# Optimization experiments

Measured on AMD Instinct MI355X. Metric: run time of the kernel, lower is better.

The kernel has to match this reference:

```python
import jax, jax.numpy as jnp
import numpy as np
from jax import lax

B, T, H = 64, 1024, 512
K = 10            # gaussian mixtures
U, V = 64, 80     # char steps, alphabet size
S = 3             # stroke dims


def setup_inputs() -> dict:
    key = jax.random.key(0)
    k1, k2, k3, k4 = jax.random.split(key, 4)
    return {
        "input0": jax.random.normal(k1, (B, T, H), dtype=jnp.float32),
        "stroke": jax.random.normal(k2, (B, T, S), dtype=jnp.float32),
        "char": jax.random.uniform(k3, (B, U, V), dtype=jnp.float32),
        "window_w": jax.random.normal(k4, (H, 3 * K), dtype=jnp.float32) * 0.05,
        "window_b": jnp.zeros((3 * K,), dtype=jnp.float32),
        "kappa0": jnp.zeros((B, K, 1), dtype=jnp.float32),
    }


def reference(input0, stroke, char, window_w, window_b, kappa0):
    u = jnp.arange(char.shape[1], dtype=input0.dtype)  # [U]
    k_mix = kappa0.shape[1]

    def step(kappa_prev, xs):
        x_t, s_t = xs  # [B,H], [B,S]
        abk = jnp.exp(x_t @ window_w + window_b)          # [B,3K]
        abk = abk.reshape(-1, 3 * k_mix, 1)               # [B,3K,1]
        alpha, beta, kappa_hat = jnp.split(abk, 3, axis=1)  # each [B,K,1]
        kappa = kappa_hat + kappa_prev                    # cumulative kappa state
        # phi_k = alpha * exp(-beta * (kappa - u)^2) -> sum over mixtures
        phi = jnp.sum(alpha * jnp.exp(-beta * jnp.square(kappa - u)), axis=1)  # [B,U]
        window = jnp.einsum('bu,buv->bv', phi, char)      # [B,V]
        out = jnp.concatenate((x_t, window, s_t), axis=1)  # [B,H+V+S]
        return kappa, out

    xs = (jnp.swapaxes(input0, 0, 1), jnp.swapaxes(stroke, 0, 1))  # [T,B,*]
    _, outs = lax.scan(step, kappa0, xs)
    return jnp.swapaxes(outs, 0, 1)  # [B,T,H+V+S]
```

## Files before the change

### kernel.cpp

```cpp
#include <hip/hip_runtime.h>

#define BB 64
#define TT 1024
#define HH 512
#define KMIX 10
#define UU 64
#define VV 80
#define SDIM 3
#define OUTW (HH + VV + SDIM)
#define ROWS 16

__global__ __launch_bounds__(256) void kW_transpose(const float* __restrict__ Wm, float* __restrict__ Wt) {
    int idx = blockIdx.x * 256 + threadIdx.x;
    if (idx < 30 * HH) {
        int j = idx >> 9, h = idx & 511;
        Wt[idx] = Wm[h * 30 + j];
    }
}

__global__ __launch_bounds__(512, 4) void k1_gemm(
    const float* __restrict__ x,
    const float* __restrict__ stroke,
    const float* __restrict__ Wt,
    const float* __restrict__ bias,
    float* __restrict__ out,
    float* __restrict__ abk)
{
    __shared__ float xs[ROWS][HH + 4];
    const int tid = threadIdx.x;
    const int r0 = blockIdx.x * ROWS;

    const float4* x4 = (const float4*)(x + (size_t)r0 * HH);
    #pragma unroll
    for (int i = 0; i < 4; ++i) {
        int f4 = tid + (i << 9);
        float4 v = x4[f4];
        *(float4*)&xs[f4 >> 7][(f4 & 127) << 2] = v;
    }
    if (tid < ROWS * SDIM) {
        int row = tid / SDIM, c = tid % SDIM;
        out[(size_t)(r0 + row) * OUTW + HH + VV + c] = stroke[(size_t)(r0 + row) * SDIM + c];
    }
    __syncthreads();

    #pragma unroll
    for (int i = 0; i < 16; ++i) {
        int idx = tid + (i << 9);
        out[(size_t)(r0 + (idx >> 9)) * OUTW + (idx & 511)] = xs[idx >> 9][idx & 511];
    }

    const bool active = tid < 480;
    float acc[ROWS];
    int j = 0, hc = 0;
    if (active) {
        hc = tid / 30;
        j = tid % 30;
        const float4* wp = (const float4*)(Wt + j * HH + hc * 32);
        float4 w4[8];
        #pragma unroll
        for (int q = 0; q < 8; ++q) w4[q] = wp[q];
        #pragma unroll
        for (int r = 0; r < ROWS; ++r) {
            const float4* xp = (const float4*)&xs[r][hc * 32];
            float s = 0.f;
            #pragma unroll
            for (int q = 0; q < 8; ++q) {
                float4 xv = xp[q];
                s += xv.x * w4[q].x + xv.y * w4[q].y + xv.z * w4[q].z + xv.w * w4[q].w;
            }
            acc[r] = s;
        }
    }
    __syncthreads();
    float* plds = &xs[0][0];
    if (active) {
        #pragma unroll
        for (int r = 0; r < ROWS; ++r) plds[r * 480 + tid] = acc[r];
    }
    __syncthreads();
    if (tid < ROWS * 30) {
        int row = tid / 30, jj = tid % 30;
        float s = 0.f;
        #pragma unroll
        for (int q = 0; q < 16; ++q) s += plds[row * 480 + q * 30 + jj];
        abk[(size_t)(r0 + row) * 30 + jj] = expf(s + bias[jj]);
    }
}

__global__ __launch_bounds__(64) void k2_scan(
    float* __restrict__ abk, const float* __restrict__ kappa0)
{
    const int b = blockIdx.x / KMIX;
    const int k = blockIdx.x % KMIX;
    const int lane = threadIdx.x;
    const size_t base = (size_t)b * TT * 30 + 20 + k;
    const int t0 = lane * 16;

    float v[16];
    #pragma unroll
    for (int i = 0; i < 16; ++i) v[i] = abk[base + (size_t)(t0 + i) * 30];
    #pragma unroll
    for (int i = 1; i < 16; ++i) v[i] += v[i - 1];

    float total = v[15];
    float xinc = total;
    #pragma unroll
    for (int off = 1; off < 64; off <<= 1) {
        float y = __shfl_up(xinc, off, 64);
        if (lane >= off) xinc += y;
    }
    float excl = xinc - total + kappa0[b * KMIX + k];

    #pragma unroll
    for (int i = 0; i < 16; ++i) abk[base + (size_t)(t0 + i) * 30] = v[i] + excl;
}

#define TCHUNK 64
__global__ __launch_bounds__(256) void k3_window(
    const float* __restrict__ abk,
    const float* __restrict__ ch,
    float* __restrict__ out)
{
    __shared__ float cs[VV][68];
    __shared__ float ab[TCHUNK][32];
    __shared__ float ph[4][64];
    const int b = blockIdx.x / (TT / TCHUNK);
    const int tc = blockIdx.x % (TT / TCHUNK);
    const int tid = threadIdx.x;
    const int wave = tid >> 6, lane = tid & 63;

    const float* cb = ch + (size_t)b * UU * VV;
    for (int i = tid; i < UU * VV; i += 256) {
        cs[i % VV][i / VV] = cb[i];
    }
    const float* ab_g = abk + (size_t)(b * TT + tc * TCHUNK) * 30;
    for (int i = tid; i < TCHUNK * 30; i += 256) {
        ab[i / 30][i % 30] = ab_g[i];
    }
    __syncthreads();

    const float uf = (float)lane;
    const float* csr1 = cs[lane];
    const float* csr2 = cs[64 + (lane & 15)];

    for (int t = wave; t < TCHUNK; t += 4) {
        float r_[32];
        #pragma unroll
        for (int q = 0; q < 8; ++q) {
            float4 v4 = *(const float4*)&ab[t][q * 4];
            r_[q * 4] = v4.x; r_[q * 4 + 1] = v4.y; r_[q * 4 + 2] = v4.z; r_[q * 4 + 3] = v4.w;
        }
        float phi = 0.f;
        #pragma unroll
        for (int k = 0; k < KMIX; ++k) {
            float d = r_[20 + k] - uf;
            phi += r_[k] * __expf(-r_[10 + k] * d * d);
        }
        ph[wave][lane] = phi;

        float acc1 = 0.f, acc2 = 0.f;
        #pragma unroll
        for (int g = 0; g < 16; ++g) {
            float4 p4 = *(const float4*)&ph[wave][g * 4];
            float4 c1 = *(const float4*)&csr1[g * 4];
            float4 c2 = *(const float4*)&csr2[g * 4];
            acc1 += p4.x * c1.x + p4.y * c1.y + p4.z * c1.z + p4.w * c1.w;
            acc2 += p4.x * c2.x + p4.y * c2.y + p4.z * c2.z + p4.w * c2.w;
        }
        float* orow = out + (size_t)(b * TT + tc * TCHUNK + t) * OUTW + HH;
        orow[lane] = acc1;
        if (lane < 16) orow[64 + lane] = acc2;
    }
}

extern "C" void kernel_launch(void* const* d_in, const int* in_sizes, int n_in,
                              void* d_out, int out_size, void* d_ws, size_t ws_size,
                              hipStream_t stream) {
    const float* input0   = (const float*)d_in[0];
    const float* stroke   = (const float*)d_in[1];
    const float* chars    = (const float*)d_in[2];
    const float* window_w = (const float*)d_in[3];
    const float* window_b = (const float*)d_in[4];
    const float* kappa0   = (const float*)d_in[5];
    float* out = (float*)d_out;
    float* abk = (float*)d_ws;
    float* Wt  = (float*)((char*)d_ws + (size_t)BB * TT * 30 * 4);

    kW_transpose<<<dim3((30 * HH + 255) / 256), dim3(256), 0, stream>>>(window_w, Wt);
    k1_gemm<<<dim3(BB * TT / ROWS), dim3(512), 0, stream>>>(input0, stroke, Wt, window_b, out, abk);
    k2_scan<<<dim3(BB * KMIX), dim3(64), 0, stream>>>(abk, kappa0);
    k3_window<<<dim3(BB * (TT / TCHUNK)), dim3(256), 0, stream>>>(abk, chars, out);
}
```

Measured before the change: 356.4 us.

## Transpose abk workspace and compute window per-timestep-per-thread with register phi

The abk workspace changes to a component-major layout, so the scan kernel can use coalesced float4 loads and stores instead of stride-30 accesses. The window kernel now gives each thread one timestep: it keeps the 64 phi values in registers, reads the transposed char matrix from LDS as broadcasts, and stages results in LDS so the output stores are coalesced. The GEMM kernel writes the x passthrough straight from the registers it just loaded, and its minimum-occupancy launch bound is dropped. The new window grid has only 256 blocks, each holding about 100KB of LDS, which risks low occupancy and poor latency hiding.

```diff
diff --git a/kernel.cpp b/kernel.cpp
--- a/kernel.cpp
+++ b/kernel.cpp
@@ -2,12 +2,13 @@
 
 #define BB 64
 #define TT 1024
+#define BT (BB * TT)
 #define HH 512
 #define KMIX 10
 #define UU 64
 #define VV 80
 #define SDIM 3
-#define OUTW (HH + VV + SDIM)
+#define OUTW 595
 #define ROWS 16
 
 __global__ __launch_bounds__(256) void kW_transpose(const float* __restrict__ Wm, float* __restrict__ Wt) {
@@ -18,13 +19,13 @@
     }
 }
 
-__global__ __launch_bounds__(512, 4) void k1_gemm(
+__global__ __launch_bounds__(512) void k1_gemm(
     const float* __restrict__ x,
     const float* __restrict__ stroke,
     const float* __restrict__ Wt,
     const float* __restrict__ bias,
     float* __restrict__ out,
-    float* __restrict__ abk)
+    float* __restrict__ abk_t)
 {
     __shared__ float xs[ROWS][HH + 4];
     const int tid = threadIdx.x;
@@ -34,8 +35,12 @@
     #pragma unroll
     for (int i = 0; i < 4; ++i) {
         int f4 = tid + (i << 9);
+        int row = f4 >> 7;
+        int col = (f4 & 127) << 2;
         float4 v = x4[f4];
-        *(float4*)&xs[f4 >> 7][(f4 & 127) << 2] = v;
+        *(float4*)&xs[row][col] = v;
+        float* orow = out + (size_t)(r0 + row) * OUTW + col;
+        orow[0] = v.x; orow[1] = v.y; orow[2] = v.z; orow[3] = v.w;
     }
     if (tid < ROWS * SDIM) {
         int row = tid / SDIM, c = tid % SDIM;
@@ -43,25 +48,17 @@
     }
     __syncthreads();
 
-    #pragma unroll
-    for (int i = 0; i < 16; ++i) {
-        int idx = tid + (i << 9);
-        out[(size_t)(r0 + (idx >> 9)) * OUTW + (idx & 511)] = xs[idx >> 9][idx & 511];
-    }
-
     const bool active = tid < 480;
     float acc[ROWS];
-    int j = 0, hc = 0;
     if (active) {
-        hc = tid / 30;
-        j = tid % 30;
+        int hc = tid / 30, j = tid % 30;
         const float4* wp = (const float4*)(Wt + j * HH + hc * 32);
         float4 w4[8];
         #pragma unroll
         for (int q = 0; q < 8; ++q) w4[q] = wp[q];
         #pragma unroll
         for (int r = 0; r < ROWS; ++r) {
-            const float4* xp = (const float4*)&xs[r][hc * 32];
+            const float4* xp = (const float4*)&xs[r][(tid / 30) * 32];
             float s = 0.f;
             #pragma unroll
             for (int q = 0; q < 8; ++q) {
@@ -78,32 +75,33 @@
         for (int r = 0; r < ROWS; ++r) plds[r * 480 + tid] = acc[r];
     }
     __syncthreads();
-    if (tid < ROWS * 30) {
-        int row = tid / 30, jj = tid % 30;
+    if (active) {
+        int row = tid & 15, jj = tid >> 4;
         float s = 0.f;
         #pragma unroll
         for (int q = 0; q < 16; ++q) s += plds[row * 480 + q * 30 + jj];
-        abk[(size_t)(r0 + row) * 30 + jj] = expf(s + bias[jj]);
+        abk_t[(size_t)jj * BT + r0 + row] = expf(s + bias[jj]);
     }
 }
 
 __global__ __launch_bounds__(64) void k2_scan(
-    float* __restrict__ abk, const float* __restrict__ kappa0)
+    float* __restrict__ abk_t, const float* __restrict__ kappa0)
 {
     const int b = blockIdx.x / KMIX;
     const int k = blockIdx.x % KMIX;
     const int lane = threadIdx.x;
-    const size_t base = (size_t)b * TT * 30 + 20 + k;
-    const int t0 = lane * 16;
+    float4* p4 = (float4*)(abk_t + (size_t)(20 + k) * BT + b * TT);
 
     float v[16];
     #pragma unroll
-    for (int i = 0; i < 16; ++i) v[i] = abk[base + (size_t)(t0 + i) * 30];
+    for (int i = 0; i < 4; ++i) {
+        float4 q = p4[lane * 4 + i];
+        v[i * 4 + 0] = q.x; v[i * 4 + 1] = q.y; v[i * 4 + 2] = q.z; v[i * 4 + 3] = q.w;
+    }
     #pragma unroll
     for (int i = 1; i < 16; ++i) v[i] += v[i - 1];
 
-    float total = v[15];
-    float xinc = total;
+    float total = v[15], xinc = total;
     #pragma unroll
     for (int off = 1; off < 64; off <<= 1) {
         float y = __shfl_up(xinc, off, 64);
@@ -112,64 +110,72 @@
     float excl = xinc - total + kappa0[b * KMIX + k];
 
     #pragma unroll
-    for (int i = 0; i < 16; ++i) abk[base + (size_t)(t0 + i) * 30] = v[i] + excl;
+    for (int i = 0; i < 4; ++i) {
+        float4 q;
+        q.x = v[i * 4 + 0] + excl; q.y = v[i * 4 + 1] + excl;
+        q.z = v[i * 4 + 2] + excl; q.w = v[i * 4 + 3] + excl;
+        p4[lane * 4 + i] = q;
+    }
 }
 
-#define TCHUNK 64
 __global__ __launch_bounds__(256) void k3_window(
-    const float* __restrict__ abk,
+    const float* __restrict__ abk_t,
     const float* __restrict__ ch,
     float* __restrict__ out)
 {
-    __shared__ float cs[VV][68];
-    __shared__ float ab[TCHUNK][32];
-    __shared__ float ph[4][64];
-    const int b = blockIdx.x / (TT / TCHUNK);
-    const int tc = blockIdx.x % (TT / TCHUNK);
+    __shared__ float cst[VV][68];
+    __shared__ float win[4][UU * 81];
+    const int b = blockIdx.x >> 2;
+    const int qtr = blockIdx.x & 3;
     const int tid = threadIdx.x;
     const int wave = tid >> 6, lane = tid & 63;
 
-    const float* cb = ch + (size_t)b * UU * VV;
-    for (int i = tid; i < UU * VV; i += 256) {
-        cs[i % VV][i / VV] = cb[i];
-    }
-    const float* ab_g = abk + (size_t)(b * TT + tc * TCHUNK) * 30;
-    for (int i = tid; i < TCHUNK * 30; i += 256) {
-        ab[i / 30][i % 30] = ab_g[i];
+    const float4* c4 = (const float4*)(ch + (size_t)b * UU * VV);
+    #pragma unroll
+    for (int i = 0; i < 5; ++i) {
+        int f4 = tid + i * 256;
+        float4 v = c4[f4];
+        int f = f4 * 4;
+        int u = f / 80;
+        int v0 = f - u * 80;
+        cst[v0][u] = v.x; cst[v0 + 1][u] = v.y; cst[v0 + 2][u] = v.z; cst[v0 + 3][u] = v.w;
     }
     __syncthreads();
 
-    const float uf = (float)lane;
-    const float* csr1 = cs[lane];
-    const float* csr2 = cs[64 + (lane & 15)];
+    const int rb = b * TT + qtr * 256 + wave * 64;
 
-    for (int t = wave; t < TCHUNK; t += 4) {
-        float r_[32];
-        #pragma unroll
-        for (int q = 0; q < 8; ++q) {
-            float4 v4 = *(const float4*)&ab[t][q * 4];
-            r_[q * 4] = v4.x; r_[q * 4 + 1] = v4.y; r_[q * 4 + 2] = v4.z; r_[q * 4 + 3] = v4.w;
-        }
-        float phi = 0.f;
+    float ab[30];
+    #pragma unroll
+    for (int j = 0; j < 30; ++j) ab[j] = abk_t[(size_t)j * BT + rb + lane];
+
+    float phi[UU];
+    #pragma unroll
+    for (int u = 0; u < UU; ++u) {
+        float s = 0.f;
+        const float uf = (float)u;
         #pragma unroll
         for (int k = 0; k < KMIX; ++k) {
-            float d = r_[20 + k] - uf;
-            phi += r_[k] * __expf(-r_[10 + k] * d * d);
+            float d = ab[20 + k] - uf;
+            s += ab[k] * __expf(-ab[10 + k] * d * d);
         }
-        ph[wave][lane] = phi;
+        phi[u] = s;
+    }
 
-        float acc1 = 0.f, acc2 = 0.f;
+    float* winw = win[wave];
+    for (int v = 0; v < VV; ++v) {
+        float a = 0.f;
         #pragma unroll
-        for (int g = 0; g < 16; ++g) {
-            float4 p4 = *(const float4*)&ph[wave][g * 4];
-            float4 c1 = *(const float4*)&csr1[g * 4];
-            float4 c2 = *(const float4*)&csr2[g * 4];
-            acc1 += p4.x * c1.x + p4.y * c1.y + p4.z * c1.z + p4.w * c1.w;
-            acc2 += p4.x * c2.x + p4.y * c2.y + p4.z * c2.z + p4.w * c2.w;
+        for (int q = 0; q < 16; ++q) {
+            float4 cq = *(const float4*)&cst[v][q * 4];
+            a += phi[q * 4 + 0] * cq.x + phi[q * 4 + 1] * cq.y
+               + phi[q * 4 + 2] * cq.z + phi[q * 4 + 3] * cq.w;
         }
-        float* orow = out + (size_t)(b * TT + tc * TCHUNK + t) * OUTW + HH;
-        orow[lane] = acc1;
-        if (lane < 16) orow[64 + lane] = acc2;
+        winw[lane * 81 + v] = a;
+    }
+
+    for (int i = lane; i < UU * VV; i += 64) {
+        int t = i / 80, v = i - t * 80;
+        out[(size_t)(rb + t) * OUTW + HH + v] = winw[t * 81 + v];
     }
 }
 
@@ -182,12 +188,12 @@
     const float* window_w = (const float*)d_in[3];
     const float* window_b = (const float*)d_in[4];
     const float* kappa0   = (const float*)d_in[5];
-    float* out = (float*)d_out;
-    float* abk = (float*)d_ws;
-    float* Wt  = (float*)((char*)d_ws + (size_t)BB * TT * 30 * 4);
+    float* out   = (float*)d_out;
+    float* abk_t = (float*)d_ws;
+    float* Wt    = (float*)((char*)d_ws + (size_t)30 * BT * 4);
 
     kW_transpose<<<dim3((30 * HH + 255) / 256), dim3(256), 0, stream>>>(window_w, Wt);
-    k1_gemm<<<dim3(BB * TT / ROWS), dim3(512), 0, stream>>>(input0, stroke, Wt, window_b, out, abk);
-    k2_scan<<<dim3(BB * KMIX), dim3(64), 0, stream>>>(abk, kappa0);
-    k3_window<<<dim3(BB * (TT / TCHUNK)), dim3(256), 0, stream>>>(abk, chars, out);
+    k1_gemm<<<dim3(BT / ROWS), dim3(512), 0, stream>>>(input0, stroke, Wt, window_b, out, abk_t);
+    k2_scan<<<dim3(BB * KMIX), dim3(64), 0, stream>>>(abk_t, kappa0);
+    k3_window<<<dim3(BB * 4), dim3(256), 0, stream>>>(abk_t, chars, out);
 }
```

Result: slower. 363.6 us (+2.0%).
